# Kernel tuning notes

Measured on AMD Instinct MI355X. Metric: run time of the kernel, lower is better.

## Reference

```python
import jax, jax.numpy as jnp
import numpy as np


def setup_inputs() -> dict:
    key = jax.random.key(0)
    k1, k2, k3, k4 = jax.random.split(key, 4)
    B, S, D_IN, D_OUT, R = 4, 2048, 4096, 4096, 8
    x = jax.random.normal(k1, (B, S, D_IN), dtype=jnp.float32)
    hra_u = jax.random.normal(k2, (D_IN, R), dtype=jnp.float32)
    base_weight = jax.random.normal(k3, (D_OUT, D_IN), dtype=jnp.float32) * 0.02
    bias = jax.random.normal(k4, (D_OUT,), dtype=jnp.float32) * 0.02
    return {"x": x, "hra_u": hra_u, "base_weight": base_weight, "bias": bias}


def reference(x, hra_u, base_weight, bias):
    # HRALinear forward (not merged, apply_GS=False):
    #   u_i = hra_u[:, i] / ||hra_u[:, i]||
    #   delta = (I - 2 u_0 u_0^T) @ ... @ (I - 2 u_{r-1} u_{r-1}^T)
    #   out = x @ (base_weight @ delta)^T + bias
    # Equivalent rank-1 form: W <- W - 2 (W u_i) u_i^T, sequentially over i.
    u = hra_u / jnp.linalg.norm(hra_u, axis=0, keepdims=True)  # [D_in, r]

    def step(W, ui):
        # W: [D_out, D_in], ui: [D_in]
        Wu = W @ ui                       # [D_out]
        return W - 2.0 * Wu[:, None] * ui[None, :], None

    new_weight, _ = jax.lax.scan(step, base_weight, u.T)  # scan over r columns
    out = jnp.einsum("bsd,od->bso", x, new_weight) + bias
    return out
```

## Files before the change

kernel.cpp:

```cpp
#include <hip/hip_runtime.h>
#include <stdint.h>

#define DIN 4096
#define DOUT 4096
#define RNK 8
#define MROWS 8192
#define NTILES 128

typedef unsigned short u16;
typedef __attribute__((ext_vector_type(8))) short short8;
typedef __attribute__((ext_vector_type(8))) unsigned short u16x8;
typedef __attribute__((ext_vector_type(4))) float f32x4;

__device__ __forceinline__ u16 f2bf(float f) {
    union { float f; uint32_t u; } v; v.f = f;
    uint32_t u = v.u;
    uint32_t r = (u + 0x7fffu + ((u >> 16) & 1u)) >> 16;
    return (u16)r;
}

__device__ __forceinline__ void gl_lds16(const u16* g, u16* lds) {
    __builtin_amdgcn_global_load_lds((const __attribute__((address_space(1))) unsigned int*)g,
                                     (__attribute__((address_space(3))) unsigned int*)lds,
                                     16, 0, 0);
}

__global__ __launch_bounds__(1024) void k_prep(const float* __restrict__ hra_u,
                                               float* __restrict__ Un,
                                               float* __restrict__ G) {
    const int t = threadIdx.x;
    float s[64];
    #pragma unroll
    for (int k = 0; k < 64; k++) s[k] = 0.f;
    for (int d = t; d < DIN; d += 1024) {
        float4 p = *(const float4*)(hra_u + d * 8);
        float4 q = *(const float4*)(hra_u + d * 8 + 4);
        float v[8] = {p.x, p.y, p.z, p.w, q.x, q.y, q.z, q.w};
        #pragma unroll
        for (int i = 0; i < 8; i++)
            #pragma unroll
            for (int j = 0; j < 8; j++)
                s[i * 8 + j] += v[i] * v[j];
    }
    #pragma unroll
    for (int k = 0; k < 64; k++)
        for (int off = 32; off; off >>= 1)
            s[k] += __shfl_down(s[k], off, 64);
    __shared__ float red[16][64];
    __shared__ float Sg[64];
    __shared__ float inv[8];
    if ((t & 63) == 0) {
        #pragma unroll
        for (int k = 0; k < 64; k++) red[t >> 6][k] = s[k];
    }
    __syncthreads();
    if (t < 64) {
        float tot = 0.f;
        #pragma unroll
        for (int w = 0; w < 16; w++) tot += red[w][t];
        Sg[t] = tot;
    }
    __syncthreads();
    if (t < 8) inv[t] = rsqrtf(Sg[t * 8 + t]);
    __syncthreads();
    if (t < 64) G[t] = Sg[t] * inv[t >> 3] * inv[t & 7];
    float iv[8];
    #pragma unroll
    for (int i = 0; i < 8; i++) iv[i] = inv[i];
    for (int d = t; d < DIN; d += 1024) {
        float4 p = *(const float4*)(hra_u + d * 8);
        float4 q = *(const float4*)(hra_u + d * 8 + 4);
        Un[0 * DIN + d] = p.x * iv[0];
        Un[1 * DIN + d] = p.y * iv[1];
        Un[2 * DIN + d] = p.z * iv[2];
        Un[3 * DIN + d] = p.w * iv[3];
        Un[4 * DIN + d] = q.x * iv[4];
        Un[5 * DIN + d] = q.y * iv[5];
        Un[6 * DIN + d] = q.z * iv[6];
        Un[7 * DIN + d] = q.w * iv[7];
    }
}

__global__ __launch_bounds__(256) void k_wy_build(const float* __restrict__ W,
                                                  const float* __restrict__ Un,
                                                  const float* __restrict__ G,
                                                  u16* __restrict__ Wb) {
    const int o = blockIdx.x;
    const int t = threadIdx.x;
    const float* wrow = W + (size_t)o * DIN;

    float4 wv[4];
    float acc[RNK] = {};
    #pragma unroll
    for (int j = 0; j < 4; j++) {
        const int c = t + j * 256;
        wv[j] = *(const float4*)(wrow + c * 4);
        #pragma unroll
        for (int i = 0; i < RNK; i++) {
            float4 uv = *(const float4*)(Un + i * DIN + c * 4);
            acc[i] += wv[j].x * uv.x + wv[j].y * uv.y + wv[j].z * uv.z + wv[j].w * uv.w;
        }
    }
    #pragma unroll
    for (int i = 0; i < RNK; i++)
        for (int off = 32; off; off >>= 1)
            acc[i] += __shfl_down(acc[i], off, 64);
    __shared__ float red[4][RNK];
    __shared__ float ysh[RNK];
    if ((t & 63) == 0) {
        #pragma unroll
        for (int i = 0; i < RNK; i++) red[t >> 6][i] = acc[i];
    }
    __syncthreads();
    if (t == 0) {
        float y[RNK];
        #pragma unroll
        for (int i = 0; i < RNK; i++) {
            float s = red[0][i] + red[1][i] + red[2][i] + red[3][i];
            for (int j = 0; j < i; j++) s -= y[j] * G[j * RNK + i];
            y[i] = 2.f * s;
            ysh[i] = y[i];
        }
    }
    __syncthreads();
    float y[RNK];
    #pragma unroll
    for (int i = 0; i < RNK; i++) y[i] = ysh[i];

    #pragma unroll
    for (int j = 0; j < 4; j++) {
        const int c = t + j * 256;
        float4 r = wv[j];
        #pragma unroll
        for (int i = 0; i < RNK; i++) {
            float4 uv = *(const float4*)(Un + i * DIN + c * 4);
            r.x -= y[i] * uv.x; r.y -= y[i] * uv.y;
            r.z -= y[i] * uv.z; r.w -= y[i] * uv.w;
        }
        ushort4 ov;
        ov.x = f2bf(r.x); ov.y = f2bf(r.y); ov.z = f2bf(r.z); ov.w = f2bf(r.w);
        *(ushort4*)(Wb + (size_t)o * DIN + c * 4) = ov;
    }
}

__global__ __launch_bounds__(256) void k_cast_x(const float* __restrict__ x,
                                                u16* __restrict__ xb) {
    const size_t total = (size_t)MROWS * DIN / 8;
    for (size_t idx = (size_t)blockIdx.x * 256 + threadIdx.x; idx < total;
         idx += (size_t)2048 * 256) {
        float4 a = *(const float4*)(x + idx * 8);
        float4 b = *(const float4*)(x + idx * 8 + 4);
        u16x8 o;
        o[0] = f2bf(a.x); o[1] = f2bf(a.y); o[2] = f2bf(a.z); o[3] = f2bf(a.w);
        o[4] = f2bf(b.x); o[5] = f2bf(b.y); o[6] = f2bf(b.z); o[7] = f2bf(b.w);
        *(u16x8*)(xb + idx * 8) = o;
    }
}

__global__ __launch_bounds__(512, 2) void k_gemm(const u16* __restrict__ A,
                                                 const u16* __restrict__ B,
                                                 const float* __restrict__ bias,
                                                 float* __restrict__ C) {
    __shared__ u16 sm[65536];

    const int t = threadIdx.x;
    const int w = t >> 6, l = t & 63;
    const int bm = blockIdx.x & 31;
    const int bn = blockIdx.x >> 5;
    const int wm = w >> 2, wn = w & 3;

    const int quad = l >> 4, lane16 = l & 15;

    const int lc   = (l & 7) ^ (l >> 3);
    const int prow = lc >> 2;
    const int kch  = lc & 3;
    const int rA0  = (2 * w) * 16 + 2 * (l >> 3) + prow;
    const u16* agp0 = A + (size_t)(bm * 256 + rA0) * DIN + kch * 8;
    const u16* agp1 = agp0 + (size_t)16 * DIN;
    const u16* bgp0 = B + (size_t)(bn * 256 + rA0) * DIN + kch * 8;
    const u16* bgp1 = bgp0 + (size_t)16 * DIN;
    const int ldso0 = (2 * w) * 512;
    const int ldso1 = (2 * w + 1) * 512;

    const int pA    = (((lane16 & 1) * 4 + quad) ^ ((lane16 >> 1) & 7)) * 8;
    const int a_off = (wm * 64 + (lane16 >> 1)) * 64 + pA;
    const int b_off = (wn * 32 + (lane16 >> 1)) * 64 + pA;

    f32x4 acc[8][4] = {};
    short8 a0[4], a1[4], bA[4], bB[4];

    #pragma unroll
    for (int tt = 0; tt < 3; tt++) {
        u16* Asw = sm + tt * 16384;
        const int kc = tt * 32;
        gl_lds16(agp0 + kc, Asw + ldso0);
        gl_lds16(agp1 + kc, Asw + ldso1);
        gl_lds16(bgp0 + kc, Asw + 8192 + ldso0);
        gl_lds16(bgp1 + kc, Asw + 8192 + ldso1);
    }
    asm volatile("s_waitcnt vmcnt(8)" ::: "memory");
    __builtin_amdgcn_s_barrier();
    #pragma unroll
    for (int mt = 0; mt < 4; mt++) a0[mt] = *(const short8*)&sm[a_off + (mt * 8) * 64];
    #pragma unroll
    for (int nt = 0; nt < 4; nt++) bA[nt] = *(const short8*)&sm[8192 + b_off + (nt * 8) * 64];

#define TILE_BODY(KT, BC, BN)                                                         \
    {                                                                                 \
        u16* As_c = sm + ((KT) & 3) * 16384;                                          \
        u16* As_n = sm + (((KT) + 1) & 3) * 16384;                                    \
        u16* As_s = sm + (((KT) + 3) & 3) * 16384;                                    \
        const int kc3 = (((KT) + 3) & (NTILES - 1)) * 32;                             \
                                     \
        _Pragma("unroll")                                                             \
        for (int mt = 0; mt < 4; mt++)                                                \
            a1[mt] = *(const short8*)&As_c[a_off + (32 + mt * 8) * 64];               \
        gl_lds16(agp0 + kc3, As_s + ldso0);                                           \
        gl_lds16(agp1 + kc3, As_s + ldso1);                                           \
        __builtin_amdgcn_sched_barrier(0);                                            \
                  \
        __builtin_amdgcn_s_setprio(1);                                                \
        _Pragma("unroll")                                                             \
        for (int mt = 0; mt < 4; mt++)                                                \
            _Pragma("unroll")                                                         \
            for (int nt = 0; nt < 4; nt++)                                            \
                acc[mt][nt] = __builtin_amdgcn_mfma_f32_16x16x32_bf16(                \
                    a0[mt], BC[nt], acc[mt][nt], 0, 0, 0);                            \
        __builtin_amdgcn_s_setprio(0);                                                \
        asm volatile("s_waitcnt vmcnt(6)" ::: "memory");                              \
        __builtin_amdgcn_s_barrier();                 \
                                         \
        _Pragma("unroll")                                                             \
        for (int mt = 0; mt < 4; mt++)                                                \
            a0[mt] = *(const short8*)&As_n[a_off + (mt * 8) * 64];                    \
        _Pragma("unroll")                                                             \
        for (int nt = 0; nt < 4; nt++)                                                \
            BN[nt] = *(const short8*)&As_n[8192 + b_off + (nt * 8) * 64];             \
        gl_lds16(bgp0 + kc3, As_s + 8192 + ldso0);                                    \
        gl_lds16(bgp1 + kc3, As_s + 8192 + ldso1);                                    \
        __builtin_amdgcn_sched_barrier(0);                                            \
                                                        \
        __builtin_amdgcn_s_setprio(1);                                                \
        _Pragma("unroll")                                                             \
        for (int mt = 0; mt < 4; mt++)                                                \
            _Pragma("unroll")                                                         \
            for (int nt = 0; nt < 4; nt++)                                            \
                acc[4 + mt][nt] = __builtin_amdgcn_mfma_f32_16x16x32_bf16(            \
                    a1[mt], BC[nt], acc[4 + mt][nt], 0, 0, 0);                        \
        __builtin_amdgcn_s_setprio(0);                                                \
    }

    #pragma unroll 1
    for (int kt2 = 0; kt2 < NTILES; kt2 += 2) {
        TILE_BODY(kt2,     bA, bB)
        TILE_BODY(kt2 + 1, bB, bA)
    }
#undef TILE_BODY

    asm volatile("s_waitcnt vmcnt(0)" ::: "memory");

    const int col0 = bn * 256 + wn * 64 + lane16;
    const int row00 = bm * 256 + wm * 128 + quad * 4;
    float bv[4];
    #pragma unroll
    for (int nt = 0; nt < 4; nt++) bv[nt] = bias[col0 + nt * 16];
    #pragma unroll
    for (int half = 0; half < 2; half++) {
        #pragma unroll
        for (int mt = 0; mt < 4; mt++) {
            const int row0 = row00 + half * 64 + mt * 16;
            #pragma unroll
            for (int nt = 0; nt < 4; nt++) {
                #pragma unroll
                for (int rr = 0; rr < 4; rr++) {
                    C[(size_t)(row0 + rr) * DOUT + col0 + nt * 16] =
                        acc[half * 4 + mt][nt][rr] + bv[nt];
                }
            }
        }
    }
}

extern "C" void kernel_launch(void* const* d_in, const int* in_sizes, int n_in,
                              void* d_out, int out_size, void* d_ws, size_t ws_size,
                              hipStream_t stream) {
    const float* x     = (const float*)d_in[0];
    const float* hra_u = (const float*)d_in[1];
    const float* W     = (const float*)d_in[2];
    const float* bias  = (const float*)d_in[3];
    float* out = (float*)d_out;

    char* ws = (char*)d_ws;
    float* Un = (float*)(ws);
    float* G  = (float*)(ws + 131072);
    u16*   Wb = (u16*)(ws + 524288);
    u16*   xb = (u16*)(ws + 524288 + 33554432);

    k_prep<<<1, 1024, 0, stream>>>(hra_u, Un, G);
    k_wy_build<<<DOUT, 256, 0, stream>>>(W, Un, G, Wb);
    k_cast_x<<<2048, 256, 0, stream>>>(x, xb);
    k_gemm<<<(MROWS / 256) * (DOUT / 256), 512, 0, stream>>>(xb, Wb, bias, out);
}
```

Measured before the change: 545.3 us.

## Fuse weight WY build with x cast and read raw hra_u with folded norms

```diff
diff --git a/kernel.cpp b/kernel.cpp
--- a/kernel.cpp
+++ b/kernel.cpp
@@ -26,8 +26,8 @@
 }
 
 __global__ __launch_bounds__(1024) void k_prep(const float* __restrict__ hra_u,
-                                               float* __restrict__ Un,
-                                               float* __restrict__ G) {
+                                               float* __restrict__ G,
+                                               float* __restrict__ INV) {
     const int t = threadIdx.x;
     float s[64];
     #pragma unroll
@@ -64,27 +64,16 @@
     if (t < 8) inv[t] = rsqrtf(Sg[t * 8 + t]);
     __syncthreads();
     if (t < 64) G[t] = Sg[t] * inv[t >> 3] * inv[t & 7];
-    float iv[8];
-    #pragma unroll
-    for (int i = 0; i < 8; i++) iv[i] = inv[i];
-    for (int d = t; d < DIN; d += 1024) {
-        float4 p = *(const float4*)(hra_u + d * 8);
-        float4 q = *(const float4*)(hra_u + d * 8 + 4);
-        Un[0 * DIN + d] = p.x * iv[0];
-        Un[1 * DIN + d] = p.y * iv[1];
-        Un[2 * DIN + d] = p.z * iv[2];
-        Un[3 * DIN + d] = p.w * iv[3];
-        Un[4 * DIN + d] = q.x * iv[4];
-        Un[5 * DIN + d] = q.y * iv[5];
-        Un[6 * DIN + d] = q.z * iv[6];
-        Un[7 * DIN + d] = q.w * iv[7];
-    }
-}
-
-__global__ __launch_bounds__(256) void k_wy_build(const float* __restrict__ W,
-                                                  const float* __restrict__ Un,
-                                                  const float* __restrict__ G,
-                                                  u16* __restrict__ Wb) {
+    if (t < 8) INV[t] = inv[t];
+}
+
+__global__ __launch_bounds__(256) void k_wy_cast(const float* __restrict__ W,
+                                                 const float* __restrict__ hra_u,
+                                                 const float* __restrict__ G,
+                                                 const float* __restrict__ INV,
+                                                 u16* __restrict__ Wb,
+                                                 const float* __restrict__ x,
+                                                 u16* __restrict__ xb) {
     const int o = blockIdx.x;
     const int t = threadIdx.x;
     const float* wrow = W + (size_t)o * DIN;
@@ -95,10 +84,16 @@
     for (int j = 0; j < 4; j++) {
         const int c = t + j * 256;
         wv[j] = *(const float4*)(wrow + c * 4);
-        #pragma unroll
-        for (int i = 0; i < RNK; i++) {
-            float4 uv = *(const float4*)(Un + i * DIN + c * 4);
-            acc[i] += wv[j].x * uv.x + wv[j].y * uv.y + wv[j].z * uv.z + wv[j].w * uv.w;
+        float wd[4] = {wv[j].x, wv[j].y, wv[j].z, wv[j].w};
+        #pragma unroll
+        for (int dd = 0; dd < 4; dd++) {
+            const int d = c * 4 + dd;
+            float4 h0 = *(const float4*)(hra_u + d * 8);
+            float4 h1 = *(const float4*)(hra_u + d * 8 + 4);
+            acc[0] += wd[dd] * h0.x; acc[1] += wd[dd] * h0.y;
+            acc[2] += wd[dd] * h0.z; acc[3] += wd[dd] * h0.w;
+            acc[4] += wd[dd] * h1.x; acc[5] += wd[dd] * h1.y;
+            acc[6] += wd[dd] * h1.z; acc[7] += wd[dd] * h1.w;
         }
     }
     #pragma unroll
@@ -106,7 +101,7 @@
         for (int off = 32; off; off >>= 1)
             acc[i] += __shfl_down(acc[i], off, 64);
     __shared__ float red[4][RNK];
-    __shared__ float ysh[RNK];
+    __shared__ float zsh[RNK];
     if ((t & 63) == 0) {
         #pragma unroll
         for (int i = 0; i < RNK; i++) red[t >> 6][i] = acc[i];
@@ -116,44 +111,43 @@
         float y[RNK];
         #pragma unroll
         for (int i = 0; i < RNK; i++) {
-            float s = red[0][i] + red[1][i] + red[2][i] + red[3][i];
+            float s = (red[0][i] + red[1][i] + red[2][i] + red[3][i]) * INV[i];
             for (int j = 0; j < i; j++) s -= y[j] * G[j * RNK + i];
             y[i] = 2.f * s;
-            ysh[i] = y[i];
-        }
-    }
-    __syncthreads();
-    float y[RNK];
-    #pragma unroll
-    for (int i = 0; i < RNK; i++) y[i] = ysh[i];
+            zsh[i] = y[i] * INV[i];
+        }
+    }
+    __syncthreads();
+    float z[RNK];
+    #pragma unroll
+    for (int i = 0; i < RNK; i++) z[i] = zsh[i];
 
     #pragma unroll
     for (int j = 0; j < 4; j++) {
         const int c = t + j * 256;
-        float4 r = wv[j];
-        #pragma unroll
-        for (int i = 0; i < RNK; i++) {
-            float4 uv = *(const float4*)(Un + i * DIN + c * 4);
-            r.x -= y[i] * uv.x; r.y -= y[i] * uv.y;
-            r.z -= y[i] * uv.z; r.w -= y[i] * uv.w;
+        float rr[4] = {wv[j].x, wv[j].y, wv[j].z, wv[j].w};
+        #pragma unroll
+        for (int dd = 0; dd < 4; dd++) {
+            const int d = c * 4 + dd;
+            float4 h0 = *(const float4*)(hra_u + d * 8);
+            float4 h1 = *(const float4*)(hra_u + d * 8 + 4);
+            rr[dd] -= z[0] * h0.x + z[1] * h0.y + z[2] * h0.z + z[3] * h0.w
+                    + z[4] * h1.x + z[5] * h1.y + z[6] * h1.z + z[7] * h1.w;
         }
         ushort4 ov;
-        ov.x = f2bf(r.x); ov.y = f2bf(r.y); ov.z = f2bf(r.z); ov.w = f2bf(r.w);
+        ov.x = f2bf(rr[0]); ov.y = f2bf(rr[1]); ov.z = f2bf(rr[2]); ov.w = f2bf(rr[3]);
         *(ushort4*)(Wb + (size_t)o * DIN + c * 4) = ov;
     }
-}
-
-__global__ __launch_bounds__(256) void k_cast_x(const float* __restrict__ x,
-                                                u16* __restrict__ xb) {
-    const size_t total = (size_t)MROWS * DIN / 8;
-    for (size_t idx = (size_t)blockIdx.x * 256 + threadIdx.x; idx < total;
-         idx += (size_t)2048 * 256) {
+
+    #pragma unroll
+    for (int it = 0; it < 4; it++) {
+        const size_t idx = (size_t)blockIdx.x * 256 + t + (size_t)it * 4096 * 256;
         float4 a = *(const float4*)(x + idx * 8);
         float4 b = *(const float4*)(x + idx * 8 + 4);
-        u16x8 o;
-        o[0] = f2bf(a.x); o[1] = f2bf(a.y); o[2] = f2bf(a.z); o[3] = f2bf(a.w);
-        o[4] = f2bf(b.x); o[5] = f2bf(b.y); o[6] = f2bf(b.z); o[7] = f2bf(b.w);
-        *(u16x8*)(xb + idx * 8) = o;
+        u16x8 ox;
+        ox[0] = f2bf(a.x); ox[1] = f2bf(a.y); ox[2] = f2bf(a.z); ox[3] = f2bf(a.w);
+        ox[4] = f2bf(b.x); ox[5] = f2bf(b.y); ox[6] = f2bf(b.z); ox[7] = f2bf(b.w);
+        *(u16x8*)(xb + idx * 8) = ox;
     }
 }
 
@@ -291,13 +285,12 @@
     float* out = (float*)d_out;
 
     char* ws = (char*)d_ws;
-    float* Un = (float*)(ws);
-    float* G  = (float*)(ws + 131072);
-    u16*   Wb = (u16*)(ws + 524288);
-    u16*   xb = (u16*)(ws + 524288 + 33554432);
-
-    k_prep<<<1, 1024, 0, stream>>>(hra_u, Un, G);
-    k_wy_build<<<DOUT, 256, 0, stream>>>(W, Un, G, Wb);
-    k_cast_x<<<2048, 256, 0, stream>>>(x, xb);
+    float* G   = (float*)(ws);
+    float* INV = (float*)(ws + 256);
+    u16*   Wb  = (u16*)(ws + 524288);
+    u16*   xb  = (u16*)(ws + 524288 + 33554432);
+
+    k_prep<<<1, 1024, 0, stream>>>(hra_u, G, INV);
+    k_wy_cast<<<DOUT, 256, 0, stream>>>(W, hra_u, G, INV, Wb, x, xb);
     k_gemm<<<(MROWS / 256) * (DOUT / 256), 512, 0, stream>>>(xb, Wb, bias, out);
 }
```

After: 618.9 us. +13.5%, slower.
